# Kernel optimization log

Hardware: AMD Instinct MI355X
Metric: run time of the kernel (lower is better)

## Reference

```python
import jax, jax.numpy as jnp
import numpy as np

H = 25  # fixed state size per module source
N_STEPS = 10


def _lstm_cell(x, h, c, W_ih, W_hh, b_ih, b_hh):
    # PyTorch LSTMCell: gates ordered i, f, g, o
    gates = x @ W_ih.T + b_ih + h @ W_hh.T + b_hh  # [B, 4H]
    i, f, g, o = jnp.split(gates, 4, axis=-1)
    c_new = jax.nn.sigmoid(f) * c + jax.nn.sigmoid(i) * jnp.tanh(g)
    h_new = jax.nn.sigmoid(o) * jnp.tanh(c_new)
    return h_new, c_new


def setup_inputs() -> dict:
    key = jax.random.key(0)
    ks = jax.random.split(key, 11)
    B, A = 131072, 18

    def u(k, shape, fan_in, fan_out):
        bound = np.sqrt(6.0 / (fan_in + fan_out)).astype(np.float32)
        return jax.random.uniform(k, shape, jnp.float32, -bound, bound)

    state = jax.random.normal(ks[0], (B, H), jnp.float32)
    # LSTMCell weights [4H, H]; biases zeroed per module init
    W_ih_enc = u(ks[1], (4 * H, H), H, 4 * H)
    W_hh_enc = u(ks[2], (4 * H, H), H, 4 * H)
    b_ih_enc = jnp.zeros((4 * H,), jnp.float32)
    b_hh_enc = jnp.zeros((4 * H,), jnp.float32)
    W_ih_dec = u(ks[3], (4 * H, H), H, 4 * H)
    W_hh_dec = u(ks[4], (4 * H, H), H, 4 * H)
    b_ih_dec = jnp.zeros((4 * H,), jnp.float32)
    b_hh_dec = jnp.zeros((4 * H,), jnp.float32)
    # actor head: norm_col_init std=0.01, bias 0
    w = jax.random.normal(ks[5], (A, H), jnp.float32)
    W_act = w * (0.01 / jnp.sqrt((w ** 2).sum(1, keepdims=True)))
    b_act = jnp.zeros((A,), jnp.float32)
    return {
        "state_repr_input": state,
        "W_ih_enc": W_ih_enc, "W_hh_enc": W_hh_enc, "b_ih_enc": b_ih_enc, "b_hh_enc": b_hh_enc,
        "W_ih_dec": W_ih_dec, "W_hh_dec": W_hh_dec, "b_ih_dec": b_ih_dec, "b_hh_dec": b_hh_dec,
        "W_act": W_act, "b_act": b_act,
    }


def reference(state_repr_input, W_ih_enc, W_hh_enc, b_ih_enc, b_hh_enc,
              W_ih_dec, W_hh_dec, b_ih_dec, b_hh_dec, W_act, b_act):
    B = state_repr_input.shape[0]
    zeros = jnp.zeros_like(state_repr_input)

    # Encoder: input to each step is previous hx (first step: state)
    def enc_step(carry, _):
        inp, h, c = carry
        h, c = _lstm_cell(inp, h, c, W_ih_enc, W_hh_enc, b_ih_enc, b_hh_enc)
        return (h, h, c), h

    (_, _, _), enc_hs = jax.lax.scan(enc_step, (state_repr_input, zeros, zeros), None, length=N_STEPS)
    # enc_hs: [10, B, 25]

    # Decoder: consumes encoder outputs in order
    def dec_step(carry, x):
        h, c = carry
        h, c = _lstm_cell(x, h, c, W_ih_dec, W_hh_dec, b_ih_dec, b_hh_dec)
        return (h, c), None

    (hx_dec, _), _ = jax.lax.scan(dec_step, (zeros, zeros), enc_hs)

    actor_lang = hx_dec @ W_act.T + b_act  # [B, A]
    return actor_lang, enc_hs
```

## Files before the change

kernel.cpp:

```cpp
#include <hip/hip_runtime.h>


#define HH 25
#define NSTEP 10
#define AOUT 18
#define WPB 8
#define BLK (WPB * 64)
#define MT 2
#define ROWS (MT * 16)
#define NFRG 34
#define FPAD 40
#define LOG2E 1.44269504088896340736f

typedef __attribute__((ext_vector_type(8))) short short8;
typedef __attribute__((ext_vector_type(4))) float f32x4;

__device__ __forceinline__ short f2bf(float x) {
    unsigned u = __float_as_uint(x);
    u += 0x7fffu + ((u >> 16) & 1u);
    return (short)(u >> 16);
}
__device__ __forceinline__ unsigned cvtpk(float lo, float hi) {
    unsigned r;
    asm("v_cvt_pk_bf16_f32 %0, %1, %2" : "=v"(r) : "v"(lo), "v"(hi));
    return r;
}
#if __has_builtin(__builtin_amdgcn_exp2f)
#define EXP2(x) __builtin_amdgcn_exp2f(x)
#else
#define EXP2(x) exp2f(x)
#endif
#define RCP(x) __builtin_amdgcn_rcpf(x)
#define MFMA16(a, b, c) __builtin_amdgcn_mfma_f32_16x16x32_bf16((a), (b), (c), 0, 0, 0)

__global__ __launch_bounds__(BLK, 4)
void langnn_mfma16(const float* __restrict__ state,
                   const float* __restrict__ Wih_e, const float* __restrict__ Whh_e,
                   const float* __restrict__ bih_e, const float* __restrict__ bhh_e,
                   const float* __restrict__ Wih_d, const float* __restrict__ Whh_d,
                   const float* __restrict__ bih_d, const float* __restrict__ bhh_d,
                   const float* __restrict__ Wact, const float* __restrict__ bact,
                   float* __restrict__ out, int B)
{
    __shared__ __align__(16) short sFrag[NFRG][64][8];
    __shared__ __align__(16) short sH[WPB][2][MT][16][FPAD];

    const int tid  = threadIdx.x;
    const int lane = tid & 63;
    const int w    = tid >> 6;
    const int r    = lane & 15;
    const int g    = lane >> 4;

    for (int i = tid; i < NFRG * 64; i += BLK) {
        const int idx = i >> 6, l = i & 63;
        const int lj = l & 15, lg = l >> 4;
        const float *W1 = nullptr, *W2 = nullptr, *B1 = nullptr, *B2 = nullptr;
        int gt = 0, jt, jmax = HH;
        if (idx < 8)       { gt = idx >> 1;        jt = idx & 1; W1 = Wih_e; W2 = Whh_e; B1 = bih_e; B2 = bhh_e; }
        else if (idx < 16) { gt = (idx - 8) >> 1;  jt = idx & 1; W1 = Wih_d; B1 = bih_d; B2 = bhh_d; }
        else if (idx < 24) { gt = (idx - 16) >> 1; jt = idx & 1; W1 = Whh_d; }
        else if (idx < 26) { jt = idx - 24;        W1 = Wact;    B1 = bact;  jmax = AOUT; }
        else               { gt = (idx - 26) >> 1; jt = idx & 1; W1 = Wih_e; B1 = bih_e; B2 = bhh_e; }
        const bool actor = (idx >= 24 && idx < 26);
        const float sc = actor ? 1.f : (gt == 2 ? 2.f * LOG2E : -LOG2E);
        const int col = jt * 16 + lj;
        const int nrow = actor ? col : gt * HH + col;
        for (int e = 0; e < 8; ++e) {
            const int k = lg * 8 + e;
            float v = 0.f;
            if (col < jmax) {
                if (k < HH) {
                    v = W1[nrow * HH + k];
                    if (W2) v += W2[nrow * HH + k];
                    v *= sc;
                } else if (k == HH && B1) {
                    v = B1[nrow];
                    if (B2) v += B2[nrow];
                    v *= sc;
                }
            }
            sFrag[idx][l][e] = f2bf(v);
        }
    }
    {
        int* z = (int*)sH;
        const int n32 = (int)(sizeof(sH) / 4);
        for (int i = tid; i < n32; i += BLK)
            z[i] = ((i % (FPAD / 2)) == 12) ? 0x3F800000 : 0;
    }
    __syncthreads();

    const int b0 = (blockIdx.x * WPB + w) * ROWS;
    float* encRow = out + (size_t)B * AOUT;

    float ce[MT][2][4], cd[MT][2][4];
    #pragma unroll
    for (int m = 0; m < MT; ++m)
        #pragma unroll
        for (int jt = 0; jt < 2; ++jt)
            #pragma unroll
            for (int q = 0; q < 4; ++q) { ce[m][jt][q] = 0.f; cd[m][jt][q] = 0.f; }

    float* pe[MT];
    #pragma unroll
    for (int m = 0; m < MT; ++m)
        pe[m] = encRow + (size_t)(b0 + m * 16 + g * 4) * HH + r;

    short8 aE[MT], aD[MT];
    #pragma unroll
    for (int m = 0; m < MT; ++m) {
        const float* sp = state + (size_t)(b0 + m * 16 + r) * HH;
        #pragma unroll
        for (int e = 0; e < 8; ++e) {
            const int k = g * 8 + e;
            aE[m][e] = (k < HH) ? f2bf(sp[k]) : (k == HH ? (short)0x3F80 : (short)0);
        }
        aD[m] = *(const short8*)&sH[w][1][m][r][g * 8];
    }

    auto encCell = [&](int fbase) {
        #pragma unroll
        for (int jt = 0; jt < 2; ++jt) {
            f32x4 acc[MT][4];
            #pragma unroll
            for (int gt = 0; gt < 4; ++gt) {
                short8 Bf = *(const short8*)&sFrag[fbase + gt * 2 + jt][lane][0];
                f32x4 z; z[0] = z[1] = z[2] = z[3] = 0.f;
                #pragma unroll
                for (int m = 0; m < MT; ++m) acc[m][gt] = MFMA16(aE[m], Bf, z);
            }
            #pragma unroll
            for (int m = 0; m < MT; ++m) {
                float hv[4];
                #pragma unroll
                for (int q = 0; q < 4; ++q) {
                    float Ei = EXP2(acc[m][0][q]);
                    float Ef = EXP2(acc[m][1][q]);
                    float Eg = EXP2(acc[m][2][q]);
                    float Eo = EXP2(acc[m][3][q]);
                    float st = (Eg - 1.f) * RCP((1.f + Ei) * (1.f + Eg));
                    float c  = fmaf(RCP(1.f + Ef), ce[m][jt][q], st);
                    ce[m][jt][q] = c;
                    float Ec = EXP2(2.f * LOG2E * c);
                    hv[q] = (Ec - 1.f) * RCP((1.f + Ec) * (1.f + Eo));
                }
                if (jt == 0 || r < 9) {
                    float* p = pe[m] + jt * 16;
                    p[0] = hv[0]; p[HH] = hv[1]; p[2 * HH] = hv[2]; p[3 * HH] = hv[3];
                    unsigned p01 = cvtpk(hv[0], hv[1]), p23 = cvtpk(hv[2], hv[3]);
                    short* sp = &sH[w][0][m][g * 4][jt * 16 + r];
                    sp[0]        = (short)p01;
                    sp[FPAD]     = (short)(p01 >> 16);
                    sp[2 * FPAD] = (short)p23;
                    sp[3 * FPAD] = (short)(p23 >> 16);
                }
            }
        }
        #pragma unroll
        for (int m = 0; m < MT; ++m) {
            aE[m] = *(const short8*)&sH[w][0][m][r][g * 8];
            pe[m] += (size_t)B * HH;
        }
    };

    auto decCell = [&]() {
        #pragma unroll
        for (int jt = 0; jt < 2; ++jt) {
            f32x4 acc[MT][4];
            #pragma unroll
            for (int gt = 0; gt < 4; ++gt) {
                short8 Bx = *(const short8*)&sFrag[8 + gt * 2 + jt][lane][0];
                short8 Bh = *(const short8*)&sFrag[16 + gt * 2 + jt][lane][0];
                f32x4 z; z[0] = z[1] = z[2] = z[3] = 0.f;
                #pragma unroll
                for (int m = 0; m < MT; ++m)
                    acc[m][gt] = MFMA16(aD[m], Bh, MFMA16(aE[m], Bx, z));
            }
            #pragma unroll
            for (int m = 0; m < MT; ++m) {
                float hv[4];
                #pragma unroll
                for (int q = 0; q < 4; ++q) {
                    float Ei = EXP2(acc[m][0][q]);
                    float Ef = EXP2(acc[m][1][q]);
                    float Eg = EXP2(acc[m][2][q]);
                    float Eo = EXP2(acc[m][3][q]);
                    float st = (Eg - 1.f) * RCP((1.f + Ei) * (1.f + Eg));
                    float c  = fmaf(RCP(1.f + Ef), cd[m][jt][q], st);
                    cd[m][jt][q] = c;
                    float Ec = EXP2(2.f * LOG2E * c);
                    hv[q] = (Ec - 1.f) * RCP((1.f + Ec) * (1.f + Eo));
                }
                if (jt == 0 || r < 9) {
                    unsigned p01 = cvtpk(hv[0], hv[1]), p23 = cvtpk(hv[2], hv[3]);
                    short* sp = &sH[w][1][m][g * 4][jt * 16 + r];
                    sp[0]        = (short)p01;
                    sp[FPAD]     = (short)(p01 >> 16);
                    sp[2 * FPAD] = (short)p23;
                    sp[3 * FPAD] = (short)(p23 >> 16);
                }
            }
        }
        #pragma unroll
        for (int m = 0; m < MT; ++m)
            aD[m] = *(const short8*)&sH[w][1][m][r][g * 8];
    };

    encCell(26);
    #pragma unroll 1
    for (int t = 0; t < NSTEP - 1; ++t) {
        decCell();
        encCell(0);
    }
    decCell();

    #pragma unroll
    for (int jt = 0; jt < 2; ++jt) {
        short8 Bf = *(const short8*)&sFrag[24 + jt][lane][0];
        #pragma unroll
        for (int m = 0; m < MT; ++m) {
            f32x4 z; z[0] = z[1] = z[2] = z[3] = 0.f;
            f32x4 o = MFMA16(aD[m], Bf, z);
            if (jt == 0 || r < 2) {
                float* p = out + (size_t)(b0 + m * 16 + g * 4) * AOUT + jt * 16 + r;
                p[0] = o[0]; p[AOUT] = o[1]; p[2 * AOUT] = o[2]; p[3 * AOUT] = o[3];
            }
        }
    }
}

extern "C" void kernel_launch(void* const* d_in, const int* in_sizes, int n_in,
                              void* d_out, int out_size, void* d_ws, size_t ws_size,
                              hipStream_t stream) {
    const float* state = (const float*)d_in[0];
    const float* Wih_e = (const float*)d_in[1];
    const float* Whh_e = (const float*)d_in[2];
    const float* bih_e = (const float*)d_in[3];
    const float* bhh_e = (const float*)d_in[4];
    const float* Wih_d = (const float*)d_in[5];
    const float* Whh_d = (const float*)d_in[6];
    const float* bih_d = (const float*)d_in[7];
    const float* bhh_d = (const float*)d_in[8];
    const float* Wact  = (const float*)d_in[9];
    const float* bact  = (const float*)d_in[10];

    int B = in_sizes[0] / HH;
    int grid = B / (WPB * ROWS);

    hipLaunchKernelGGL(langnn_mfma16, dim3(grid), dim3(BLK), 0, stream,
                       state, Wih_e, Whh_e, bih_e, bhh_e,
                       Wih_d, Whh_d, bih_d, bhh_d, Wact, bact,
                       (float*)d_out, B);
}
```

Baseline: 97.69 us.

## Drop per-wave row tiling to one 16-row tile and reuse sH for first-step weights

Each wave now handles 16 batch rows instead of 32, which halves per-thread accumulator and cell-state registers and doubles the grid; launch bounds are raised to target 6 waves' worth of occupancy. The first-encoder-step weight fragments are staged temporarily in the decoder half of the sH buffer rather than in dedicated sFrag slots, shrinking LDS, with an extra block barrier and re-zeroing before the decoder starts. The gate math is also algebraically restructured to use one fewer reciprocal per element. The trade-off is less MFMA interleaving per wave (less ILP to hide MFMA and transcendental latency) and duplicated weight-fragment setup across twice as many blocks.

```diff
diff --git a/kernel.cpp b/kernel.cpp
--- a/kernel.cpp
+++ b/kernel.cpp
@@ -6,9 +6,7 @@
 #define AOUT 18
 #define WPB 8
 #define BLK (WPB * 64)
-#define MT 2
-#define ROWS (MT * 16)
-#define NFRG 34
+#define NFRG 26
 #define FPAD 40
 #define LOG2E 1.44269504088896340736f
 
@@ -33,7 +31,7 @@
 #define RCP(x) __builtin_amdgcn_rcpf(x)
 #define MFMA16(a, b, c) __builtin_amdgcn_mfma_f32_16x16x32_bf16((a), (b), (c), 0, 0, 0)
 
-__global__ __launch_bounds__(BLK, 4)
+__global__ __launch_bounds__(BLK, 6)
 void langnn_mfma16(const float* __restrict__ state,
                    const float* __restrict__ Wih_e, const float* __restrict__ Whh_e,
                    const float* __restrict__ bih_e, const float* __restrict__ bhh_e,
@@ -43,7 +41,7 @@
                    float* __restrict__ out, int B)
 {
     __shared__ __align__(16) short sFrag[NFRG][64][8];
-    __shared__ __align__(16) short sH[WPB][2][MT][16][FPAD];
+    __shared__ __align__(16) short sH[2][WPB][16][FPAD];
 
     const int tid  = threadIdx.x;
     const int lane = tid & 63;
@@ -59,9 +57,8 @@
         if (idx < 8)       { gt = idx >> 1;        jt = idx & 1; W1 = Wih_e; W2 = Whh_e; B1 = bih_e; B2 = bhh_e; }
         else if (idx < 16) { gt = (idx - 8) >> 1;  jt = idx & 1; W1 = Wih_d; B1 = bih_d; B2 = bhh_d; }
         else if (idx < 24) { gt = (idx - 16) >> 1; jt = idx & 1; W1 = Whh_d; }
-        else if (idx < 26) { jt = idx - 24;        W1 = Wact;    B1 = bact;  jmax = AOUT; }
-        else               { gt = (idx - 26) >> 1; jt = idx & 1; W1 = Wih_e; B1 = bih_e; B2 = bhh_e; }
-        const bool actor = (idx >= 24 && idx < 26);
+        else               { jt = idx - 24;        W1 = Wact;    B1 = bact;  jmax = AOUT; }
+        const bool actor = (idx >= 24);
         const float sc = actor ? 1.f : (gt == 2 ? 2.f * LOG2E : -LOG2E);
         const int col = jt * 16 + lj;
         const int nrow = actor ? col : gt * HH + col;
@@ -83,148 +80,152 @@
         }
     }
     {
-        int* z = (int*)sH;
-        const int n32 = (int)(sizeof(sH) / 4);
-        for (int i = tid; i < n32; i += BLK)
+        short* W0 = &sH[1][0][0][0];
+        for (int i = tid; i < 8 * 64; i += BLK) {
+            const int idx = i >> 6, l = i & 63;
+            const int lj = l & 15, lg = l >> 4;
+            const int gt = idx >> 1, jt = idx & 1;
+            const float sc = (gt == 2 ? 2.f * LOG2E : -LOG2E);
+            const int col = jt * 16 + lj;
+            const int nrow = gt * HH + col;
+            for (int e = 0; e < 8; ++e) {
+                const int k = lg * 8 + e;
+                float v = 0.f;
+                if (col < HH) {
+                    if (k < HH)       v = Wih_e[nrow * HH + k] * sc;
+                    else if (k == HH) v = (bih_e[nrow] + bhh_e[nrow]) * sc;
+                }
+                W0[(size_t)idx * 512 + l * 8 + e] = f2bf(v);
+            }
+        }
+    }
+    {
+        int* z = (int*)&sH[0][0][0][0];
+        for (int i = tid; i < WPB * 16 * (FPAD / 2); i += BLK)
             z[i] = ((i % (FPAD / 2)) == 12) ? 0x3F800000 : 0;
     }
     __syncthreads();
 
-    const int b0 = (blockIdx.x * WPB + w) * ROWS;
-    float* encRow = out + (size_t)B * AOUT;
-
-    float ce[MT][2][4], cd[MT][2][4];
+    const int b0 = (blockIdx.x * WPB + w) * 16;
+    float* pe = out + (size_t)B * AOUT + (size_t)(b0 + g * 4) * HH + r;
+
+    float ce[2][4], cd[2][4];
     #pragma unroll
-    for (int m = 0; m < MT; ++m)
-        #pragma unroll
-        for (int jt = 0; jt < 2; ++jt)
-            #pragma unroll
-            for (int q = 0; q < 4; ++q) { ce[m][jt][q] = 0.f; cd[m][jt][q] = 0.f; }
-
-    float* pe[MT];
-    #pragma unroll
-    for (int m = 0; m < MT; ++m)
-        pe[m] = encRow + (size_t)(b0 + m * 16 + g * 4) * HH + r;
-
-    short8 aE[MT], aD[MT];
-    #pragma unroll
-    for (int m = 0; m < MT; ++m) {
-        const float* sp = state + (size_t)(b0 + m * 16 + r) * HH;
+    for (int jt = 0; jt < 2; ++jt)
+        #pragma unroll
+        for (int q = 0; q < 4; ++q) { ce[jt][q] = 0.f; cd[jt][q] = 0.f; }
+
+    short8 aE, aD;
+    {
+        const float* sp0 = state + (size_t)(b0 + r) * HH;
         #pragma unroll
         for (int e = 0; e < 8; ++e) {
             const int k = g * 8 + e;
-            aE[m][e] = (k < HH) ? f2bf(sp[k]) : (k == HH ? (short)0x3F80 : (short)0);
-        }
-        aD[m] = *(const short8*)&sH[w][1][m][r][g * 8];
-    }
-
-    auto encCell = [&](int fbase) {
+            aE[e] = (k < HH) ? f2bf(sp0[k]) : (k == HH ? (short)0x3F80 : (short)0);
+            aD[e] = (k == HH) ? (short)0x3F80 : (short)0;
+        }
+    }
+
+    auto encCell = [&](const short (*FB)[64][8]) {
         #pragma unroll
         for (int jt = 0; jt < 2; ++jt) {
-            f32x4 acc[MT][4];
+            f32x4 acc[4];
             #pragma unroll
             for (int gt = 0; gt < 4; ++gt) {
-                short8 Bf = *(const short8*)&sFrag[fbase + gt * 2 + jt][lane][0];
+                short8 Bf = *(const short8*)&FB[gt * 2 + jt][lane][0];
                 f32x4 z; z[0] = z[1] = z[2] = z[3] = 0.f;
-                #pragma unroll
-                for (int m = 0; m < MT; ++m) acc[m][gt] = MFMA16(aE[m], Bf, z);
-            }
-            #pragma unroll
-            for (int m = 0; m < MT; ++m) {
-                float hv[4];
-                #pragma unroll
-                for (int q = 0; q < 4; ++q) {
-                    float Ei = EXP2(acc[m][0][q]);
-                    float Ef = EXP2(acc[m][1][q]);
-                    float Eg = EXP2(acc[m][2][q]);
-                    float Eo = EXP2(acc[m][3][q]);
-                    float st = (Eg - 1.f) * RCP((1.f + Ei) * (1.f + Eg));
-                    float c  = fmaf(RCP(1.f + Ef), ce[m][jt][q], st);
-                    ce[m][jt][q] = c;
-                    float Ec = EXP2(2.f * LOG2E * c);
-                    hv[q] = (Ec - 1.f) * RCP((1.f + Ec) * (1.f + Eo));
-                }
-                if (jt == 0 || r < 9) {
-                    float* p = pe[m] + jt * 16;
-                    p[0] = hv[0]; p[HH] = hv[1]; p[2 * HH] = hv[2]; p[3 * HH] = hv[3];
-                    unsigned p01 = cvtpk(hv[0], hv[1]), p23 = cvtpk(hv[2], hv[3]);
-                    short* sp = &sH[w][0][m][g * 4][jt * 16 + r];
-                    sp[0]        = (short)p01;
-                    sp[FPAD]     = (short)(p01 >> 16);
-                    sp[2 * FPAD] = (short)p23;
-                    sp[3 * FPAD] = (short)(p23 >> 16);
-                }
-            }
-        }
-        #pragma unroll
-        for (int m = 0; m < MT; ++m) {
-            aE[m] = *(const short8*)&sH[w][0][m][r][g * 8];
-            pe[m] += (size_t)B * HH;
-        }
+                acc[gt] = MFMA16(aE, Bf, z);
+            }
+            float hv[4];
+            #pragma unroll
+            for (int q = 0; q < 4; ++q) {
+                float Ei = EXP2(acc[0][q]);
+                float Ef = EXP2(acc[1][q]);
+                float Eg = EXP2(acc[2][q]);
+                float Eo = EXP2(acc[3][q]);
+                float Pf = 1.f + Ef;
+                float Pig = (1.f + Ei) * (1.f + Eg);
+                float c = fmaf(ce[jt][q], Pig, (Eg - 1.f) * Pf) * RCP(Pf * Pig);
+                ce[jt][q] = c;
+                float Ec = EXP2(2.f * LOG2E * c);
+                float Pc = 1.f + Ec;
+                hv[q] = (Pc - 2.f) * RCP(Pc * (1.f + Eo));
+            }
+            if (jt == 0 || r < 9) {
+                float* p = pe + jt * 16;
+                p[0] = hv[0]; p[HH] = hv[1]; p[2 * HH] = hv[2]; p[3 * HH] = hv[3];
+                unsigned p01 = cvtpk(hv[0], hv[1]), p23 = cvtpk(hv[2], hv[3]);
+                short* sp = &sH[0][w][g * 4][jt * 16 + r];
+                sp[0]        = (short)p01;
+                sp[FPAD]     = (short)(p01 >> 16);
+                sp[2 * FPAD] = (short)p23;
+                sp[3 * FPAD] = (short)(p23 >> 16);
+            }
+        }
+        aE = *(const short8*)&sH[0][w][r][g * 8];
+        pe += (size_t)B * HH;
     };
 
     auto decCell = [&]() {
         #pragma unroll
         for (int jt = 0; jt < 2; ++jt) {
-            f32x4 acc[MT][4];
+            f32x4 acc[4];
             #pragma unroll
             for (int gt = 0; gt < 4; ++gt) {
                 short8 Bx = *(const short8*)&sFrag[8 + gt * 2 + jt][lane][0];
                 short8 Bh = *(const short8*)&sFrag[16 + gt * 2 + jt][lane][0];
                 f32x4 z; z[0] = z[1] = z[2] = z[3] = 0.f;
-                #pragma unroll
-                for (int m = 0; m < MT; ++m)
-                    acc[m][gt] = MFMA16(aD[m], Bh, MFMA16(aE[m], Bx, z));
-            }
-            #pragma unroll
-            for (int m = 0; m < MT; ++m) {
-                float hv[4];
-                #pragma unroll
-                for (int q = 0; q < 4; ++q) {
-                    float Ei = EXP2(acc[m][0][q]);
-                    float Ef = EXP2(acc[m][1][q]);
-                    float Eg = EXP2(acc[m][2][q]);
-                    float Eo = EXP2(acc[m][3][q]);
-                    float st = (Eg - 1.f) * RCP((1.f + Ei) * (1.f + Eg));
-                    float c  = fmaf(RCP(1.f + Ef), cd[m][jt][q], st);
-                    cd[m][jt][q] = c;
-                    float Ec = EXP2(2.f * LOG2E * c);
-                    hv[q] = (Ec - 1.f) * RCP((1.f + Ec) * (1.f + Eo));
-                }
-                if (jt == 0 || r < 9) {
-                    unsigned p01 = cvtpk(hv[0], hv[1]), p23 = cvtpk(hv[2], hv[3]);
-                    short* sp = &sH[w][1][m][g * 4][jt * 16 + r];
-                    sp[0]        = (short)p01;
-                    sp[FPAD]     = (short)(p01 >> 16);
-                    sp[2 * FPAD] = (short)p23;
-                    sp[3 * FPAD] = (short)(p23 >> 16);
-                }
-            }
-        }
-        #pragma unroll
-        for (int m = 0; m < MT; ++m)
-            aD[m] = *(const short8*)&sH[w][1][m][r][g * 8];
+                acc[gt] = MFMA16(aD, Bh, MFMA16(aE, Bx, z));
+            }
+            float hv[4];
+            #pragma unroll
+            for (int q = 0; q < 4; ++q) {
+                float Ei = EXP2(acc[0][q]);
+                float Ef = EXP2(acc[1][q]);
+                float Eg = EXP2(acc[2][q]);
+                float Eo = EXP2(acc[3][q]);
+                float Pf = 1.f + Ef;
+                float Pig = (1.f + Ei) * (1.f + Eg);
+                float c = fmaf(cd[jt][q], Pig, (Eg - 1.f) * Pf) * RCP(Pf * Pig);
+                cd[jt][q] = c;
+                float Ec = EXP2(2.f * LOG2E * c);
+                float Pc = 1.f + Ec;
+                hv[q] = (Pc - 2.f) * RCP(Pc * (1.f + Eo));
+            }
+            if (jt == 0 || r < 9) {
+                unsigned p01 = cvtpk(hv[0], hv[1]), p23 = cvtpk(hv[2], hv[3]);
+                short* sp = &sH[1][w][g * 4][jt * 16 + r];
+                sp[0]        = (short)p01;
+                sp[FPAD]     = (short)(p01 >> 16);
+                sp[2 * FPAD] = (short)p23;
+                sp[3 * FPAD] = (short)(p23 >> 16);
+            }
+        }
+        aD = *(const short8*)&sH[1][w][r][g * 8];
     };
 
-    encCell(26);
+    encCell((const short (*)[64][8])&sH[1][0][0][0]);
+    __syncthreads();
+    {
+        int* z = (int*)&sH[1][w][0][0];
+        for (int i = lane; i < 16 * (FPAD / 2); i += 64)
+            z[i] = ((i % (FPAD / 2)) == 12) ? 0x3F800000 : 0;
+    }
+    decCell();
     #pragma unroll 1
-    for (int t = 0; t < NSTEP - 1; ++t) {
+    for (int t = 1; t < NSTEP; ++t) {
+        encCell(sFrag);
         decCell();
-        encCell(0);
-    }
-    decCell();
+    }
 
     #pragma unroll
     for (int jt = 0; jt < 2; ++jt) {
         short8 Bf = *(const short8*)&sFrag[24 + jt][lane][0];
-        #pragma unroll
-        for (int m = 0; m < MT; ++m) {
-            f32x4 z; z[0] = z[1] = z[2] = z[3] = 0.f;
-            f32x4 o = MFMA16(aD[m], Bf, z);
-            if (jt == 0 || r < 2) {
-                float* p = out + (size_t)(b0 + m * 16 + g * 4) * AOUT + jt * 16 + r;
-                p[0] = o[0]; p[AOUT] = o[1]; p[2 * AOUT] = o[2]; p[3 * AOUT] = o[3];
-            }
+        f32x4 z; z[0] = z[1] = z[2] = z[3] = 0.f;
+        f32x4 o = MFMA16(aD, Bf, z);
+        if (jt == 0 || r < 2) {
+            float* p = out + (size_t)(b0 + g * 4) * AOUT + jt * 16 + r;
+            p[0] = o[0]; p[AOUT] = o[1]; p[2 * AOUT] = o[2]; p[3 * AOUT] = o[3];
         }
     }
 }
@@ -245,7 +246,7 @@
     const float* bact  = (const float*)d_in[10];
 
     int B = in_sizes[0] / HH;
-    int grid = B / (WPB * ROWS);
+    int grid = B / (WPB * 16);
 
     hipLaunchKernelGGL(langnn_mfma16, dim3(grid), dim3(BLK), 0, stream,
                        state, Wih_e, Whh_e, bih_e, bhh_e,
```

Result: slower. 188.8 us (+93.3%).
